# Kernel tuning notes

Measured on AMD Instinct MI355X. Metric: run time of the kernel, lower is better.

## Reference

```python
import jax, jax.numpy as jnp
import numpy as np

H = 16
D = 1024
DK = D // H
DFF = 2048


def _layernorm(x, g, b, eps=1e-6):
    # Faithful to source: uses Bessel-corrected std (torch .std default) and (std + eps)
    m = x.mean(-1, keepdims=True)
    s = jnp.std(x, axis=-1, keepdims=True, ddof=1)
    return g * (x - m) / (s + eps) + b


def _mha(q_in, k_in, v_in, wq, bq, wk, bk, wv, bv, wo, bo, causal):
    B, Tq, _ = q_in.shape
    def proj(x, w, bb):
        y = x @ w + bb                          # [B, T, D]
        return y.reshape(B, -1, H, DK).transpose(0, 2, 1, 3)  # [B, H, T, dk]
    q = proj(q_in, wq, bq)
    k = proj(k_in, wk, bk)
    v = proj(v_in, wv, bv)
    scores = jnp.einsum('bhqd,bhkd->bhqk', q, k) / jnp.sqrt(jnp.float32(DK))
    if causal:
        Tk = k.shape[2]
        mask = jnp.tril(jnp.ones((Tq, Tk), dtype=bool))  # allowed positions
        scores = jnp.where(mask, scores, -jnp.inf)
    p = jax.nn.softmax(scores, axis=-1)
    out = jnp.einsum('bhqk,bhkd->bhqd', p, v)
    out = out.transpose(0, 2, 1, 3).reshape(B, Tq, D)
    return out @ wo + bo, p


def setup_inputs() -> dict:
    key = jax.random.key(0)
    ks = jax.random.split(key, 16)
    B, T, HC, WC = 16, 512, 32, 32
    s = 0.02
    inp = {
        'text': jax.random.normal(ks[0], (B, T, D), jnp.float32),
        'conv_feature': jax.random.normal(ks[1], (B, D, HC, WC), jnp.float32),
    }
    # masked self-attention params
    for i, nm in enumerate(['sa_wq', 'sa_wk', 'sa_wv', 'sa_wo']):
        inp[nm] = jax.random.normal(ks[2 + i], (D, D), jnp.float32) * s
        inp[nm.replace('w', 'b')] = jnp.zeros((D,), jnp.float32)
    # cross-attention params
    for i, nm in enumerate(['ca_wq', 'ca_wk', 'ca_wv', 'ca_wo']):
        inp[nm] = jax.random.normal(ks[6 + i], (D, D), jnp.float32) * s
        inp[nm.replace('w', 'b')] = jnp.zeros((D,), jnp.float32)
    # FFN params
    inp['ffn_w1'] = jax.random.normal(ks[10], (D, DFF), jnp.float32) * s
    inp['ffn_b1'] = jnp.zeros((DFF,), jnp.float32)
    inp['ffn_w2'] = jax.random.normal(ks[11], (DFF, D), jnp.float32) * s
    inp['ffn_b2'] = jnp.zeros((D,), jnp.float32)
    # LayerNorm params
    for i in (1, 2, 3):
        inp[f'ln{i}_g'] = jnp.ones((D,), jnp.float32)
        inp[f'ln{i}_b'] = jnp.zeros((D,), jnp.float32)
    return inp


def reference(text, conv_feature,
              sa_wq, sa_bq, sa_wk, sa_bk, sa_wv, sa_bv, sa_wo, sa_bo,
              ca_wq, ca_bq, ca_wk, ca_bk, ca_wv, ca_bv, ca_wo, ca_bo,
              ffn_w1, ffn_b1, ffn_w2, ffn_b2,
              ln1_g, ln1_b, ln2_g, ln2_b, ln3_g, ln3_b):
    # masked (causal) self-attention + residual + LN
    sa_out, _ = _mha(text, text, text,
                     sa_wq, sa_bq, sa_wk, sa_bk, sa_wv, sa_bv, sa_wo, sa_bo,
                     causal=True)
    result = _layernorm(text + sa_out, ln1_g, ln1_b)
    # conv feature map [B, C, h, w] -> [B, h*w, C]
    B, C, h, w = conv_feature.shape
    kv = conv_feature.reshape(B, C, h * w).transpose(0, 2, 1)
    # cross-attention + residual + LN
    ca_out, attn_map = _mha(result, kv, kv,
                            ca_wq, ca_bq, ca_wk, ca_bk, ca_wv, ca_bv, ca_wo, ca_bo,
                            causal=False)
    result = _layernorm(result + ca_out, ln2_g, ln2_b)
    # FFN + residual + LN (dropout inactive at inference)
    ffn = jax.nn.relu(result @ ffn_w1 + ffn_b1) @ ffn_w2 + ffn_b2
    result = _layernorm(result + ffn, ln3_g, ln3_b)
    return result, attn_map
```

## Files before the change

kernel.cpp:

```cpp
#include <hip/hip_runtime.h>

#define DEV __device__ __forceinline__

typedef unsigned short u16;
typedef __attribute__((ext_vector_type(8))) short short8;
typedef __attribute__((ext_vector_type(4))) float f32x4;

DEV u16 f2b(float f) {
  union { float f; unsigned u; } x; x.f = f;
  unsigned r = x.u + 0x7fffu + ((x.u >> 16) & 1u);
  return (u16)(r >> 16);
}
DEV float b2f(u16 h) { union { unsigned u; float f; } x; x.u = ((unsigned)h) << 16; return x.f; }
DEV float tof(float v) { return v; }
DEV float tof(u16 v) { return b2f(v); }
DEV void stf(float* p, float v) { *p = v; }
DEV void stf(u16* p, float v) { *p = f2b(v); }

DEV void async_ld16(const void* g, void* l) {
  __builtin_amdgcn_global_load_lds(
      (const __attribute__((address_space(1))) void*)g,
      (__attribute__((address_space(3))) void*)l, 16, 0, 0);
}

template <int BM, int BN, bool AF32>
__launch_bounds__(256, 2)
__global__ void gemm_bt(const void* __restrict__ Ap, const u16* __restrict__ Btp,
                        float* __restrict__ Cf, u16* __restrict__ Cb,
                        const float* __restrict__ bias, const float* __restrict__ Res,
                        int K, int lda, int ldb, int ldc, int Hd,
                        long sAo, long sAi, long sBo, long sBi, long sCo, long sCi,
                        float scale, int relu) {
  constexpr int BK = 32;
  __shared__ __align__(16) u16 lA[BM * BK];
  __shared__ __align__(16) u16 lB[BN * BK];
  const int z = blockIdx.z;
  const long aoff = (long)(z / Hd) * sAo + (long)(z % Hd) * sAi;
  const long boff = (long)(z / Hd) * sBo + (long)(z % Hd) * sBi;
  const long coff = (long)(z / Hd) * sCo + (long)(z % Hd) * sCi;
  const u16* A16 = (const u16*)Ap + aoff;
  const float* A32 = (const float*)Ap + aoff;
  const u16* Bt = Btp + boff;

  const int m0 = blockIdx.y * BM;
  const int n0 = blockIdx.x * BN;
  const int tid = threadIdx.x;
  const int lane = tid & 63;
  const int wave = tid >> 6;
  const int wr = wave >> 1, wc = wave & 1;
  constexpr int WM = BM / 2, WN = BN / 2;
  constexpr int MI = WM / 16, NI = WN / 16;
  constexpr int ISS_A = BM / 64;
  constexpr int ISS_B = BN / 64;

  f32x4 acc[MI][NI];
#pragma unroll
  for (int i = 0; i < MI; ++i)
#pragma unroll
    for (int j = 0; j < NI; ++j) acc[i][j] = {0.f, 0.f, 0.f, 0.f};

  const int rl = lane & 15;
  const int kq = (lane >> 4) * 8;

  for (int kt = 0; kt < K; kt += BK) {
    if (kt) __syncthreads();
    if (!AF32) {
#pragma unroll
      for (int i = 0; i < ISS_A; ++i) {
        int chunk = (wave * ISS_A + i) * 64 + lane;
        int r = chunk >> 2, c = (chunk & 3) * 8;
        async_ld16(A16 + (long)(m0 + r) * lda + kt + c,
                   (char*)lA + (wave * ISS_A + i) * 1024);
      }
    } else {
#pragma unroll
      for (int i = 0; i < (BM * BK) / 1024; ++i) {
        int e = (i * 256 + tid) * 4;
        int r = e >> 5, c = e & 31;
        float4 v = *(const float4*)(A32 + (long)(m0 + r) * lda + kt + c);
        ushort4 pk;
        pk.x = f2b(v.x); pk.y = f2b(v.y); pk.z = f2b(v.z); pk.w = f2b(v.w);
        *(ushort4*)(lA + r * BK + c) = pk;
      }
    }
#pragma unroll
    for (int i = 0; i < ISS_B; ++i) {
      int chunk = (wave * ISS_B + i) * 64 + lane;
      int r = chunk >> 2, c = (chunk & 3) * 8;
      async_ld16(Bt + (long)(n0 + r) * ldb + kt + c,
                 (char*)lB + (wave * ISS_B + i) * 1024);
    }
    __syncthreads();

    short8 af[MI], bfr[NI];
#pragma unroll
    for (int mi = 0; mi < MI; ++mi)
      af[mi] = *(const short8*)(lA + (wr * WM + mi * 16 + rl) * BK + kq);
#pragma unroll
    for (int ni = 0; ni < NI; ++ni)
      bfr[ni] = *(const short8*)(lB + (wc * WN + ni * 16 + rl) * BK + kq);
#pragma unroll
    for (int mi = 0; mi < MI; ++mi)
#pragma unroll
      for (int ni = 0; ni < NI; ++ni)
        acc[mi][ni] = __builtin_amdgcn_mfma_f32_16x16x32_bf16(af[mi], bfr[ni], acc[mi][ni], 0, 0, 0);
  }

  const int rq = (lane >> 4) * 4;
#pragma unroll
  for (int mi = 0; mi < MI; ++mi) {
#pragma unroll
    for (int ni = 0; ni < NI; ++ni) {
      int gc = n0 + wc * WN + ni * 16 + rl;
      float bv = bias ? bias[gc] : 0.f;
#pragma unroll
      for (int r = 0; r < 4; ++r) {
        int gr = m0 + wr * WM + mi * 16 + rq + r;
        long ci = coff + (long)gr * ldc + gc;
        float v = acc[mi][ni][r] * scale + bv;
        if (Res) v += Res[ci];
        if (relu) v = fmaxf(v, 0.f);
        if (Cf) Cf[ci] = v;
        if (Cb) Cb[ci] = f2b(v);
      }
    }
  }
}

template <typename SRC>
__launch_bounds__(256)
__global__ void transpose_cvt(const SRC* __restrict__ in, u16* __restrict__ out,
                              int R, int C, int ldin, int Hd, long so, long si, long oz) {
  __shared__ float tile[32][33];
  int z = blockIdx.z;
  long ib = (long)(z / Hd) * so + (long)(z % Hd) * si;
  int r0 = blockIdx.y * 32, c0 = blockIdx.x * 32;
  int tx = threadIdx.x & 31, ty = threadIdx.x >> 5;
#pragma unroll
  for (int i = 0; i < 32; i += 8)
    tile[ty + i][tx] = tof(in[ib + (long)(r0 + ty + i) * ldin + (c0 + tx)]);
  __syncthreads();
  long ob = (long)z * oz;
#pragma unroll
  for (int i = 0; i < 32; i += 8)
    out[ob + (long)(c0 + ty + i) * R + (r0 + tx)] = f2b(tile[tx][ty + i]);
}

__launch_bounds__(256)
__global__ void cvt_f32_bf16(const float* __restrict__ in, u16* __restrict__ out) {
  long i = ((long)blockIdx.x * 256 + threadIdx.x) * 4;
  float4 v = *(const float4*)(in + i);
  ushort4 o;
  o.x = f2b(v.x); o.y = f2b(v.y); o.z = f2b(v.z); o.w = f2b(v.w);
  *(ushort4*)(out + i) = o;
}

template <typename TIO>
__launch_bounds__(256)
__global__ void softmax_rows(TIO* __restrict__ p, int len, int qmask, float scale, int causal) {
  int row = blockIdx.x * 4 + (threadIdx.x >> 6);
  int lane = threadIdx.x & 63;
  TIO* pr = p + (long)row * len;
  int q = row & qmask;
  float vals[16];
  int n = len >> 6;
  float mx = -1e30f;
  for (int i = 0; i < n; ++i) {
    int e = lane + (i << 6);
    float v = tof(pr[e]) * scale;
    if (causal && e > q) v = -1e30f;
    vals[i] = v;
    mx = fmaxf(mx, v);
  }
#pragma unroll
  for (int o = 32; o; o >>= 1) mx = fmaxf(mx, __shfl_xor(mx, o));
  float s = 0.f;
  for (int i = 0; i < n; ++i) { vals[i] = __expf(vals[i] - mx); s += vals[i]; }
#pragma unroll
  for (int o = 32; o; o >>= 1) s += __shfl_xor(s, o);
  float inv = 1.f / s;
  for (int i = 0; i < n; ++i) stf(&pr[lane + (i << 6)], vals[i] * inv);
}

__launch_bounds__(256)
__global__ void ln_rows(const float* __restrict__ x, const float* __restrict__ g,
                        const float* __restrict__ b, float* __restrict__ outf,
                        u16* __restrict__ outb) {
  __shared__ float red[8];
  int row = blockIdx.x, tid = threadIdx.x;
  int lane = tid & 63, wave = tid >> 6;
  const float4 v = *(const float4*)(x + (long)row * 1024 + tid * 4);
  float s = v.x + v.y + v.z + v.w;
#pragma unroll
  for (int o = 32; o; o >>= 1) s += __shfl_xor(s, o);
  if (lane == 0) red[wave] = s;
  __syncthreads();
  float mean = (red[0] + red[1] + red[2] + red[3]) * (1.f / 1024.f);
  float4 d;
  d.x = v.x - mean; d.y = v.y - mean; d.z = v.z - mean; d.w = v.w - mean;
  float sq = d.x * d.x + d.y * d.y + d.z * d.z + d.w * d.w;
#pragma unroll
  for (int o = 32; o; o >>= 1) sq += __shfl_xor(sq, o);
  if (lane == 0) red[4 + wave] = sq;
  __syncthreads();
  float var = (red[4] + red[5] + red[6] + red[7]) * (1.f / 1023.f);
  float inv = 1.f / (sqrtf(var) + 1e-6f);
  const float4 gv = *(const float4*)(g + tid * 4);
  const float4 bv = *(const float4*)(b + tid * 4);
  float4 y;
  y.x = gv.x * d.x * inv + bv.x;
  y.y = gv.y * d.y * inv + bv.y;
  y.z = gv.z * d.z * inv + bv.z;
  y.w = gv.w * d.w * inv + bv.w;
  if (outf) *(float4*)(outf + (long)row * 1024 + tid * 4) = y;
  if (outb) {
    ushort4 o;
    o.x = f2b(y.x); o.y = f2b(y.y); o.z = f2b(y.z); o.w = f2b(y.w);
    *(ushort4*)(outb + (long)row * 1024 + tid * 4) = o;
  }
}

extern "C" void kernel_launch(void* const* d_in, const int* in_sizes, int n_in,
                              void* d_out, int out_size, void* d_ws, size_t ws_size,
                              hipStream_t stream) {
  const float* text   = (const float*)d_in[0];
  const float* conv   = (const float*)d_in[1];
  const float* sa_wq  = (const float*)d_in[2];
  const float* sa_bq  = (const float*)d_in[3];
  const float* sa_wk  = (const float*)d_in[4];
  const float* sa_bk  = (const float*)d_in[5];
  const float* sa_wv  = (const float*)d_in[6];
  const float* sa_bv  = (const float*)d_in[7];
  const float* sa_wo  = (const float*)d_in[8];
  const float* sa_bo  = (const float*)d_in[9];
  const float* ca_wq  = (const float*)d_in[10];
  const float* ca_bq  = (const float*)d_in[11];
  const float* ca_wk  = (const float*)d_in[12];
  const float* ca_bk  = (const float*)d_in[13];
  const float* ca_wv  = (const float*)d_in[14];
  const float* ca_bv  = (const float*)d_in[15];
  const float* ca_wo  = (const float*)d_in[16];
  const float* ca_bo  = (const float*)d_in[17];
  const float* ffn_w1 = (const float*)d_in[18];
  const float* ffn_b1 = (const float*)d_in[19];
  const float* ffn_w2 = (const float*)d_in[20];
  const float* ffn_b2 = (const float*)d_in[21];
  const float* ln1_g  = (const float*)d_in[22];
  const float* ln1_b  = (const float*)d_in[23];
  const float* ln2_g  = (const float*)d_in[24];
  const float* ln2_b  = (const float*)d_in[25];
  const float* ln3_g  = (const float*)d_in[26];
  const float* ln3_b  = (const float*)d_in[27];

  char* ws = (char*)d_ws;
  const size_t MiB = 1u << 20;
  u16* wt_saq = (u16*)(ws + 0 * MiB);
  u16* wt_sak = (u16*)(ws + 2 * MiB);
  u16* wt_sav = (u16*)(ws + 4 * MiB);
  u16* wt_sao = (u16*)(ws + 6 * MiB);
  u16* wt_caq = (u16*)(ws + 8 * MiB);
  u16* wt_cak = (u16*)(ws + 10 * MiB);
  u16* wt_cav = (u16*)(ws + 12 * MiB);
  u16* wt_cao = (u16*)(ws + 14 * MiB);
  u16* wt_f1  = (u16*)(ws + 16 * MiB);
  u16* wt_f2  = (u16*)(ws + 20 * MiB);
  u16* XB    = (u16*)(ws + 24 * MiB);
  u16* ATTNB = XB;
  u16* QB    = (u16*)(ws + 40 * MiB);
  u16* RES1B = QB;
  u16* KB    = (u16*)(ws + 56 * MiB);
  u16* Q2B   = KB;
  u16* VB    = (u16*)(ws + 72 * MiB);
  u16* CAB   = VB;
  u16* VT    = (u16*)(ws + 88 * MiB);
  u16* RES2B = VT;
  u16* PB    = (u16*)(ws + 104 * MiB);
  u16* KVB   = (u16*)(ws + 104 * MiB);
  u16* K2B   = (u16*)(ws + 136 * MiB);
  u16* V2B   = (u16*)(ws + 168 * MiB);
  u16* VT2   = (u16*)(ws + 200 * MiB);
  float* BUF  = (float*)(ws + 232 * MiB);
  u16*   HID  = (u16*)(ws + 264 * MiB);
  float* RES1 = (float*)(ws + 296 * MiB);
  float* RES2 = RES1;
  float* result = (float*)d_out;
  float* pmap   = (float*)d_out + 8388608;

  dim3 tb(256);

  cvt_f32_bf16<<<8192, tb, 0, stream>>>(text, XB);
  transpose_cvt<float><<<dim3(32, 32, 1), tb, 0, stream>>>(sa_wq, wt_saq, 1024, 1024, 1024, 1, 0, 0, 0);
  transpose_cvt<float><<<dim3(32, 32, 1), tb, 0, stream>>>(sa_wk, wt_sak, 1024, 1024, 1024, 1, 0, 0, 0);
  transpose_cvt<float><<<dim3(32, 32, 1), tb, 0, stream>>>(sa_wv, wt_sav, 1024, 1024, 1024, 1, 0, 0, 0);
  transpose_cvt<float><<<dim3(32, 32, 1), tb, 0, stream>>>(sa_wo, wt_sao, 1024, 1024, 1024, 1, 0, 0, 0);
  transpose_cvt<float><<<dim3(32, 32, 1), tb, 0, stream>>>(ca_wq, wt_caq, 1024, 1024, 1024, 1, 0, 0, 0);
  transpose_cvt<float><<<dim3(32, 32, 1), tb, 0, stream>>>(ca_wk, wt_cak, 1024, 1024, 1024, 1, 0, 0, 0);
  transpose_cvt<float><<<dim3(32, 32, 1), tb, 0, stream>>>(ca_wv, wt_cav, 1024, 1024, 1024, 1, 0, 0, 0);
  transpose_cvt<float><<<dim3(32, 32, 1), tb, 0, stream>>>(ca_wo, wt_cao, 1024, 1024, 1024, 1, 0, 0, 0);
  transpose_cvt<float><<<dim3(64, 32, 1), tb, 0, stream>>>(ffn_w1, wt_f1, 1024, 2048, 2048, 1, 0, 0, 0);
  transpose_cvt<float><<<dim3(32, 64, 1), tb, 0, stream>>>(ffn_w2, wt_f2, 2048, 1024, 1024, 1, 0, 0, 0);

  gemm_bt<128, 128, false><<<dim3(8, 64, 1), tb, 0, stream>>>(
      XB, wt_saq, nullptr, QB, sa_bq, nullptr, 1024, 1024, 1024, 1024, 1, 0, 0, 0, 0, 0, 0, 1.f, 0);
  gemm_bt<128, 128, false><<<dim3(8, 64, 1), tb, 0, stream>>>(
      XB, wt_sak, nullptr, KB, sa_bk, nullptr, 1024, 1024, 1024, 1024, 1, 0, 0, 0, 0, 0, 0, 1.f, 0);
  gemm_bt<128, 128, false><<<dim3(8, 64, 1), tb, 0, stream>>>(
      XB, wt_sav, nullptr, VB, sa_bv, nullptr, 1024, 1024, 1024, 1024, 1, 0, 0, 0, 0, 0, 0, 1.f, 0);
  transpose_cvt<u16><<<dim3(2, 16, 256), tb, 0, stream>>>(VB, VT, 512, 64, 1024, 16, 524288, 64, 32768);
  gemm_bt<128, 128, false><<<dim3(4, 4, 256), tb, 0, stream>>>(
      QB, KB, nullptr, PB, nullptr, nullptr, 64, 1024, 1024, 512, 16,
      524288, 64, 524288, 64, 4194304, 262144, 1.f, 0);
  softmax_rows<u16><<<32768, tb, 0, stream>>>(PB, 512, 511, 0.125f, 1);
  gemm_bt<128, 64, false><<<dim3(1, 4, 256), tb, 0, stream>>>(
      PB, VT, nullptr, ATTNB, nullptr, nullptr, 512, 512, 512, 1024, 16,
      4194304, 262144, 524288, 32768, 524288, 64, 1.f, 0);
  gemm_bt<128, 128, false><<<dim3(8, 64, 1), tb, 0, stream>>>(
      ATTNB, wt_sao, BUF, nullptr, sa_bo, text, 1024, 1024, 1024, 1024, 1, 0, 0, 0, 0, 0, 0, 1.f, 0);
  ln_rows<<<8192, tb, 0, stream>>>(BUF, ln1_g, ln1_b, RES1, RES1B);

  transpose_cvt<float><<<dim3(32, 32, 16), tb, 0, stream>>>(conv, KVB, 1024, 1024, 1024, 1, 1048576, 0, 1048576);
  gemm_bt<128, 128, false><<<dim3(8, 64, 1), tb, 0, stream>>>(
      RES1B, wt_caq, nullptr, Q2B, ca_bq, nullptr, 1024, 1024, 1024, 1024, 1, 0, 0, 0, 0, 0, 0, 1.f, 0);
  gemm_bt<128, 128, false><<<dim3(8, 128, 1), tb, 0, stream>>>(
      KVB, wt_cak, nullptr, K2B, ca_bk, nullptr, 1024, 1024, 1024, 1024, 1, 0, 0, 0, 0, 0, 0, 1.f, 0);
  gemm_bt<128, 128, false><<<dim3(8, 128, 1), tb, 0, stream>>>(
      KVB, wt_cav, nullptr, V2B, ca_bv, nullptr, 1024, 1024, 1024, 1024, 1, 0, 0, 0, 0, 0, 0, 1.f, 0);
  transpose_cvt<u16><<<dim3(2, 32, 256), tb, 0, stream>>>(V2B, VT2, 1024, 64, 1024, 16, 1048576, 64, 65536);
  gemm_bt<128, 128, false><<<dim3(8, 4, 256), tb, 0, stream>>>(
      Q2B, K2B, pmap, nullptr, nullptr, nullptr, 64, 1024, 1024, 1024, 16,
      524288, 64, 1048576, 64, 8388608, 524288, 1.f, 0);
  softmax_rows<float><<<32768, tb, 0, stream>>>(pmap, 1024, 511, 0.125f, 0);
  gemm_bt<128, 64, true><<<dim3(1, 4, 256), tb, 0, stream>>>(
      pmap, VT2, nullptr, CAB, nullptr, nullptr, 1024, 1024, 1024, 1024, 16,
      8388608, 524288, 1048576, 65536, 524288, 64, 1.f, 0);
  gemm_bt<128, 128, false><<<dim3(8, 64, 1), tb, 0, stream>>>(
      CAB, wt_cao, BUF, nullptr, ca_bo, RES1, 1024, 1024, 1024, 1024, 1, 0, 0, 0, 0, 0, 0, 1.f, 0);
  ln_rows<<<8192, tb, 0, stream>>>(BUF, ln2_g, ln2_b, RES2, RES2B);

  gemm_bt<128, 128, false><<<dim3(16, 64, 1), tb, 0, stream>>>(
      RES2B, wt_f1, nullptr, HID, ffn_b1, nullptr, 1024, 1024, 1024, 2048, 1, 0, 0, 0, 0, 0, 0, 1.f, 1);
  gemm_bt<128, 128, false><<<dim3(8, 64, 1), tb, 0, stream>>>(
      HID, wt_f2, BUF, nullptr, ffn_b2, RES2, 2048, 2048, 2048, 1024, 1, 0, 0, 0, 0, 0, 0, 1.f, 0);
  ln_rows<<<8192, tb, 0, stream>>>(BUF, ln3_g, ln3_b, result, nullptr);
}
```

Measured before the change: 1.894 ms.

## Fuse QK^T, softmax and PV into a two-pass flash-style attention kernel

Replaces the three-kernel attention sequence (score GEMM, row softmax, PV GEMM) for both self- and cross-attention with one fused kernel. The first pass computes row max and sum over K chunks, and the second recomputes scores, normalizes them, optionally writes the fp32 probability map, and accumulates P·V from LDS. This removes the HBM round trip of the bf16/fp32 score matrices and the separate softmax pass, and the causal path skips masked chunks. In exchange QK^T is computed twice, there are more barriers, and the grid drops to 1024 blocks. The cross-attention probability map still has to be written to global memory.

```diff
diff --git a/kernel.cpp b/kernel.cpp
--- a/kernel.cpp
+++ b/kernel.cpp
@@ -14,8 +14,6 @@
 DEV float b2f(u16 h) { union { unsigned u; float f; } x; x.u = ((unsigned)h) << 16; return x.f; }
 DEV float tof(float v) { return v; }
 DEV float tof(u16 v) { return b2f(v); }
-DEV void stf(float* p, float v) { *p = v; }
-DEV void stf(u16* p, float v) { *p = f2b(v); }
 
 DEV void async_ld16(const void* g, void* l) {
   __builtin_amdgcn_global_load_lds(
@@ -127,6 +125,204 @@
   }
 }
 
+template <int TK, bool CAUSAL, bool WP>
+__launch_bounds__(256, 2)
+__global__ void attn_fused(const u16* __restrict__ Qp, const u16* __restrict__ Kp,
+                           const u16* __restrict__ Vtp, float* __restrict__ Pp,
+                           u16* __restrict__ Op) {
+  __shared__ __align__(16) u16 lQ[128 * 64];
+  __shared__ __align__(16) u16 lK[128 * 64];
+  __shared__ __align__(16) u16 lVt[64 * 128];
+  __shared__ __align__(16) u16 lP[4][32 * 128];
+
+  const int bh = blockIdx.y, b = bh >> 4, h = bh & 15;
+  const u16* Qb = Qp + (long)b * 524288 + h * 64;
+  const u16* Kb = Kp + (long)b * ((long)TK * 1024) + h * 64;
+  const u16* Vtb = Vtp + (long)bh * (64L * TK);
+  float* Pb = Pp ? Pp + (long)b * (16L * 512 * TK) + (long)h * (512L * TK) : nullptr;
+  u16* Ob = Op + (long)b * 524288 + h * 64;
+
+  const int q0 = blockIdx.x * 128;
+  const int tid = threadIdx.x, lane = tid & 63, wave = tid >> 6;
+  const int rl = lane & 15;
+  const int cbase = (lane >> 4) * 16;
+  const int rq = (lane >> 4) * 4;
+  const int w32 = wave * 32;
+  const int nch = CAUSAL ? (blockIdx.x + 1) : (TK / 128);
+
+#pragma unroll
+  for (int i = 0; i < 4; ++i) {
+    int base = (wave * 4 + i) * 1024;
+    int p = base + lane * 16;
+    int row = p >> 7;
+    int col = ((p ^ ((row & 7) << 4)) & 127) >> 1;
+    async_ld16(Qb + (long)(q0 + row) * 1024 + col, (char*)lQ + base);
+  }
+
+  auto stageK = [&](int kt) {
+#pragma unroll
+    for (int i = 0; i < 4; ++i) {
+      int base = (wave * 4 + i) * 1024;
+      int p = base + lane * 16;
+      int row = p >> 7;
+      int col = ((p ^ ((row & 7) << 4)) & 127) >> 1;
+      async_ld16(Kb + (long)(kt + row) * 1024 + col, (char*)lK + base);
+    }
+  };
+  auto computeS = [&](f32x4 (&s)[2][8]) {
+#pragma unroll
+    for (int mi = 0; mi < 2; ++mi)
+#pragma unroll
+      for (int ni = 0; ni < 8; ++ni) s[mi][ni] = {0.f, 0.f, 0.f, 0.f};
+#pragma unroll
+    for (int kk = 0; kk < 2; ++kk) {
+      const int cb = kk * 64 + cbase;
+      short8 aq[2], bk[8];
+#pragma unroll
+      for (int mi = 0; mi < 2; ++mi) {
+        int rr = w32 + mi * 16 + rl;
+        aq[mi] = *(const short8*)((const char*)lQ + ((((rr << 7) + cb)) ^ ((rr & 7) << 4)));
+      }
+#pragma unroll
+      for (int ni = 0; ni < 8; ++ni) {
+        int rr = ni * 16 + rl;
+        bk[ni] = *(const short8*)((const char*)lK + ((((rr << 7) + cb)) ^ ((rr & 7) << 4)));
+      }
+#pragma unroll
+      for (int mi = 0; mi < 2; ++mi)
+#pragma unroll
+        for (int ni = 0; ni < 8; ++ni)
+          s[mi][ni] = __builtin_amdgcn_mfma_f32_16x16x32_bf16(aq[mi], bk[ni], s[mi][ni], 0, 0, 0);
+    }
+  };
+
+  float m_[2][4], l_[2][4];
+#pragma unroll
+  for (int mi = 0; mi < 2; ++mi)
+#pragma unroll
+    for (int r = 0; r < 4; ++r) { m_[mi][r] = -1e30f; l_[mi][r] = 0.f; }
+
+  for (int c = 0; c < nch; ++c) {
+    const int kt = c * 128;
+    if (c) __syncthreads();
+    stageK(kt);
+    __syncthreads();
+
+    f32x4 s[2][8];
+    computeS(s);
+#pragma unroll
+    for (int mi = 0; mi < 2; ++mi)
+#pragma unroll
+      for (int r = 0; r < 4; ++r) {
+        int gq = q0 + w32 + mi * 16 + rq + r;
+        float vv[8];
+        float mx = -1e30f;
+#pragma unroll
+        for (int ni = 0; ni < 8; ++ni) {
+          float v = s[mi][ni][r] * 0.125f;
+          if (CAUSAL && (kt + ni * 16 + rl > gq)) v = -1e30f;
+          vv[ni] = v;
+          mx = fmaxf(mx, v);
+        }
+#pragma unroll
+        for (int o = 8; o; o >>= 1) mx = fmaxf(mx, __shfl_xor(mx, o));
+        float mo = m_[mi][r], mn = fmaxf(mo, mx);
+        float sum = 0.f;
+#pragma unroll
+        for (int ni = 0; ni < 8; ++ni) sum += __expf(vv[ni] - mn);
+#pragma unroll
+        for (int o = 8; o; o >>= 1) sum += __shfl_xor(sum, o);
+        l_[mi][r] = l_[mi][r] * __expf(mo - mn) + sum;
+        m_[mi][r] = mn;
+      }
+  }
+
+  float il[2][4];
+#pragma unroll
+  for (int mi = 0; mi < 2; ++mi)
+#pragma unroll
+    for (int r = 0; r < 4; ++r) il[mi][r] = 1.f / l_[mi][r];
+
+  f32x4 o_[2][4];
+#pragma unroll
+  for (int mi = 0; mi < 2; ++mi)
+#pragma unroll
+    for (int nj = 0; nj < 4; ++nj) o_[mi][nj] = {0.f, 0.f, 0.f, 0.f};
+
+  __syncthreads();
+
+  u16* lPw = &lP[wave][0];
+  for (int c = 0; c < nch; ++c) {
+    const int kt = c * 128;
+    if (c) __syncthreads();
+    stageK(kt);
+#pragma unroll
+    for (int i = 0; i < 4; ++i) {
+      int base = (wave * 4 + i) * 1024;
+      int p = base + lane * 16;
+      int row = p >> 8;
+      int col = ((p ^ ((row & 7) << 4)) & 255) >> 1;
+      async_ld16(Vtb + (long)row * TK + kt + col, (char*)lVt + base);
+    }
+    __syncthreads();
+
+    f32x4 s[2][8];
+    computeS(s);
+
+#pragma unroll
+    for (int mi = 0; mi < 2; ++mi)
+#pragma unroll
+      for (int r = 0; r < 4; ++r) {
+        int prow = mi * 16 + rq + r;
+        int gq = q0 + w32 + prow;
+        float mm = m_[mi][r], ii = il[mi][r];
+#pragma unroll
+        for (int ni = 0; ni < 8; ++ni) {
+          int col = ni * 16 + rl;
+          float v = s[mi][ni][r] * 0.125f;
+          if (CAUSAL && (kt + col > gq)) v = -1e30f;
+          float p = __expf(v - mm) * ii;
+          if constexpr (WP) Pb[(long)gq * TK + kt + col] = p;
+          *(u16*)((char*)lPw + (((prow << 8) + col * 2) ^ ((prow & 7) << 4))) = f2b(p);
+        }
+      }
+    __syncthreads();
+
+#pragma unroll
+    for (int kk = 0; kk < 4; ++kk) {
+      const int cb = kk * 64 + cbase;
+      short8 ap[2], bv[4];
+#pragma unroll
+      for (int mi = 0; mi < 2; ++mi) {
+        int rr = mi * 16 + rl;
+        ap[mi] = *(const short8*)((const char*)lPw + ((((rr << 8) + cb)) ^ ((rr & 7) << 4)));
+      }
+#pragma unroll
+      for (int nj = 0; nj < 4; ++nj) {
+        int rr = nj * 16 + rl;
+        bv[nj] = *(const short8*)((const char*)lVt + ((((rr << 8) + cb)) ^ ((rr & 7) << 4)));
+      }
+#pragma unroll
+      for (int mi = 0; mi < 2; ++mi)
+#pragma unroll
+        for (int nj = 0; nj < 4; ++nj)
+          o_[mi][nj] = __builtin_amdgcn_mfma_f32_16x16x32_bf16(ap[mi], bv[nj], o_[mi][nj], 0, 0, 0);
+    }
+  }
+
+#pragma unroll
+  for (int mi = 0; mi < 2; ++mi)
+#pragma unroll
+    for (int nj = 0; nj < 4; ++nj) {
+      int dk = nj * 16 + rl;
+#pragma unroll
+      for (int r = 0; r < 4; ++r) {
+        int gq = q0 + w32 + mi * 16 + rq + r;
+        Ob[(long)gq * 1024 + dk] = f2b(o_[mi][nj][r]);
+      }
+    }
+}
+
 template <typename SRC>
 __launch_bounds__(256)
 __global__ void transpose_cvt(const SRC* __restrict__ in, u16* __restrict__ out,
@@ -153,33 +349,6 @@
   ushort4 o;
   o.x = f2b(v.x); o.y = f2b(v.y); o.z = f2b(v.z); o.w = f2b(v.w);
   *(ushort4*)(out + i) = o;
-}
-
-template <typename TIO>
-__launch_bounds__(256)
-__global__ void softmax_rows(TIO* __restrict__ p, int len, int qmask, float scale, int causal) {
-  int row = blockIdx.x * 4 + (threadIdx.x >> 6);
-  int lane = threadIdx.x & 63;
-  TIO* pr = p + (long)row * len;
-  int q = row & qmask;
-  float vals[16];
-  int n = len >> 6;
-  float mx = -1e30f;
-  for (int i = 0; i < n; ++i) {
-    int e = lane + (i << 6);
-    float v = tof(pr[e]) * scale;
-    if (causal && e > q) v = -1e30f;
-    vals[i] = v;
-    mx = fmaxf(mx, v);
-  }
-#pragma unroll
-  for (int o = 32; o; o >>= 1) mx = fmaxf(mx, __shfl_xor(mx, o));
-  float s = 0.f;
-  for (int i = 0; i < n; ++i) { vals[i] = __expf(vals[i] - mx); s += vals[i]; }
-#pragma unroll
-  for (int o = 32; o; o >>= 1) s += __shfl_xor(s, o);
-  float inv = 1.f / s;
-  for (int i = 0; i < n; ++i) stf(&pr[lane + (i << 6)], vals[i] * inv);
 }
 
 __launch_bounds__(256)
@@ -274,7 +443,6 @@
   u16* CAB   = VB;
   u16* VT    = (u16*)(ws + 88 * MiB);
   u16* RES2B = VT;
-  u16* PB    = (u16*)(ws + 104 * MiB);
   u16* KVB   = (u16*)(ws + 104 * MiB);
   u16* K2B   = (u16*)(ws + 136 * MiB);
   u16* V2B   = (u16*)(ws + 168 * MiB);
@@ -307,13 +475,7 @@
   gemm_bt<128, 128, false><<<dim3(8, 64, 1), tb, 0, stream>>>(
       XB, wt_sav, nullptr, VB, sa_bv, nullptr, 1024, 1024, 1024, 1024, 1, 0, 0, 0, 0, 0, 0, 1.f, 0);
   transpose_cvt<u16><<<dim3(2, 16, 256), tb, 0, stream>>>(VB, VT, 512, 64, 1024, 16, 524288, 64, 32768);
-  gemm_bt<128, 128, false><<<dim3(4, 4, 256), tb, 0, stream>>>(
-      QB, KB, nullptr, PB, nullptr, nullptr, 64, 1024, 1024, 512, 16,
-      524288, 64, 524288, 64, 4194304, 262144, 1.f, 0);
-  softmax_rows<u16><<<32768, tb, 0, stream>>>(PB, 512, 511, 0.125f, 1);
-  gemm_bt<128, 64, false><<<dim3(1, 4, 256), tb, 0, stream>>>(
-      PB, VT, nullptr, ATTNB, nullptr, nullptr, 512, 512, 512, 1024, 16,
-      4194304, 262144, 524288, 32768, 524288, 64, 1.f, 0);
+  attn_fused<512, true, false><<<dim3(4, 256), tb, 0, stream>>>(QB, KB, VT, nullptr, ATTNB);
   gemm_bt<128, 128, false><<<dim3(8, 64, 1), tb, 0, stream>>>(
       ATTNB, wt_sao, BUF, nullptr, sa_bo, text, 1024, 1024, 1024, 1024, 1, 0, 0, 0, 0, 0, 0, 1.f, 0);
   ln_rows<<<8192, tb, 0, stream>>>(BUF, ln1_g, ln1_b, RES1, RES1B);
@@ -326,13 +488,7 @@
   gemm_bt<128, 128, false><<<dim3(8, 128, 1), tb, 0, stream>>>(
       KVB, wt_cav, nullptr, V2B, ca_bv, nullptr, 1024, 1024, 1024, 1024, 1, 0, 0, 0, 0, 0, 0, 1.f, 0);
   transpose_cvt<u16><<<dim3(2, 32, 256), tb, 0, stream>>>(V2B, VT2, 1024, 64, 1024, 16, 1048576, 64, 65536);
-  gemm_bt<128, 128, false><<<dim3(8, 4, 256), tb, 0, stream>>>(
-      Q2B, K2B, pmap, nullptr, nullptr, nullptr, 64, 1024, 1024, 1024, 16,
-      524288, 64, 1048576, 64, 8388608, 524288, 1.f, 0);
-  softmax_rows<float><<<32768, tb, 0, stream>>>(pmap, 1024, 511, 0.125f, 0);
-  gemm_bt<128, 64, true><<<dim3(1, 4, 256), tb, 0, stream>>>(
-      pmap, VT2, nullptr, CAB, nullptr, nullptr, 1024, 1024, 1024, 1024, 16,
-      8388608, 524288, 1048576, 65536, 524288, 64, 1.f, 0);
+  attn_fused<1024, false, true><<<dim3(4, 256), tb, 0, stream>>>(Q2B, K2B, VT2, pmap, CAB);
   gemm_bt<128, 128, false><<<dim3(8, 64, 1), tb, 0, stream>>>(
       CAB, wt_cao, BUF, nullptr, ca_bo, RES1, 1024, 1024, 1024, 1024, 1, 0, 0, 0, 0, 0, 0, 1.f, 0);
   ln_rows<<<8192, tb, 0, stream>>>(BUF, ln2_g, ln2_b, RES2, RES2B);
```

Measured after the change: 1.590 ms. 1.19x faster.
